# Optimization experiments

Measured on AMD Instinct MI355X. Metric: run time of the kernel, lower is better.

The kernel has to match this reference:

```python
import jax, jax.numpy as jnp
import numpy as np

COMMITMENT_COST = 0.25
NUM_EMBEDDINGS = 1024
EMBEDDING_DIM = 256


def setup_inputs() -> dict:
    key = jax.random.key(0)
    k1, k2 = jax.random.split(key)
    inputs = jax.random.normal(k1, (16, 4096, EMBEDDING_DIM), dtype=jnp.float32)
    # codebook initialized uniform(-1/K, 1/K) as in the torch module
    embeddings = jax.random.uniform(
        k2, (NUM_EMBEDDINGS, EMBEDDING_DIM), dtype=jnp.float32,
        minval=-1.0 / NUM_EMBEDDINGS, maxval=1.0 / NUM_EMBEDDINGS)
    return {"inputs": inputs, "embeddings": embeddings}


def reference(inputs, embeddings):
    sg = jax.lax.stop_gradient
    D = embeddings.shape[1]
    input_shape = inputs.shape
    flat = sg(inputs).reshape(-1, D)  # [N, D]
    distances = (jnp.sum(embeddings ** 2, axis=1)
                 + jnp.sum(flat ** 2, axis=1, keepdims=True)
                 - 2.0 * jnp.matmul(flat, embeddings.T))  # [N, K]
    indices = jnp.argmin(distances, axis=-1)  # [N]
    quantized = embeddings[indices].reshape(input_shape)
    e_latent_loss = jnp.mean((sg(quantized) - inputs) ** 2)
    q_latent_loss = jnp.mean((quantized - sg(inputs)) ** 2)
    loss = q_latent_loss + COMMITMENT_COST * e_latent_loss
    # straight-through estimator
    quantized = inputs + sg(quantized - inputs)
    return loss, quantized
```

## Files before the change

kernel.cpp:

```cpp
#include <hip/hip_runtime.h>
#include <math.h>

#define DIM 256
#define KCODES 1024
#define NTILE 64
#define BM 128
#define EB 4096.0f
#define UNIT_SCALE 0x7F7F7F7F

typedef __attribute__((ext_vector_type(8))) int i32x8;
typedef __attribute__((ext_vector_type(4))) int i32x4;
typedef __attribute__((ext_vector_type(4))) float f32x4;

__device__ inline unsigned fp4q(float v) {
  const float a = fabsf(v);
  const unsigned s = (v < 0.0f) ? 8u : 0u;
  unsigned m;
  if (a < 0.25f) m = 0;
  else if (a < 0.75f) m = 1;
  else if (a < 1.25f) m = 2;
  else if (a < 1.75f) m = 3;
  else if (a < 2.5f) m = 4;
  else if (a < 3.5f) m = 5;
  else if (a < 5.0f) m = 6;
  else m = 7;
  return s | m;
}

__global__ __launch_bounds__(64) void vq_prep_kernel(
    const float* __restrict__ E, float* __restrict__ enormh,
    unsigned char* __restrict__ Ef4) {
  const int k = blockIdx.x;
  const int t = threadIdx.x;
  const float4 v = *reinterpret_cast<const float4*>(&E[k * DIM + t * 4]);
  const int d0 = t * 4;
  const size_t byte = (size_t)((k >> 4) * 2048) + (size_t)((d0 >> 7) * 1024) +
                      (size_t)(((((d0 >> 5) & 3) * 16) + (k & 15)) * 16) +
                      (size_t)((d0 & 31) >> 1);
  const unsigned n0 = fp4q(v.x * EB), n1 = fp4q(v.y * EB);
  const unsigned n2 = fp4q(v.z * EB), n3 = fp4q(v.w * EB);
  const unsigned short pk =
      (unsigned short)(n0 | (n1 << 4) | (n2 << 8) | (n3 << 12));
  *reinterpret_cast<unsigned short*>(Ef4 + byte) = pk;
  float s = v.x * v.x + v.y * v.y + v.z * v.z + v.w * v.w;
#pragma unroll
  for (int off = 32; off >= 1; off >>= 1) s += __shfl_down(s, off);
  if (t == 0) enormh[k] = -0.5f * EB * s;
}

__global__ __launch_bounds__(256, 2) void vq_fused_kernel(
    const float* __restrict__ X, const float* __restrict__ E,
    const unsigned char* __restrict__ Ef4, const float* __restrict__ enormh,
    float* __restrict__ outq, float* __restrict__ partials) {
  __shared__ int idxs[BM];
  __shared__ float lred[4];

  const int tid = threadIdx.x;
  const int w = tid >> 6;
  const int lane = tid & 63;
  const int lr = lane & 15;
  const int lk = lane >> 4;
  const int row0 = blockIdx.x * BM;

  i32x8 Af[2][2];
  float xsq = 0.0f;
#pragma unroll
  for (int mt = 0; mt < 2; ++mt) {
    const float* xrow = &X[(size_t)(row0 + w * 32 + mt * 16 + lr) * DIM];
#pragma unroll
    for (int ks2 = 0; ks2 < 2; ++ks2) {
      const int k0 = ks2 * 128 + lk * 32;
      i32x8 af;
#pragma unroll
      for (int p = 0; p < 8; ++p) {
        const float4 a = *reinterpret_cast<const float4*>(&xrow[k0 + p * 4]);
        xsq += a.x * a.x + a.y * a.y + a.z * a.z + a.w * a.w;
        int pk = __builtin_amdgcn_cvt_pk_fp8_f32(a.x, a.y, 0, 0);
        pk = __builtin_amdgcn_cvt_pk_fp8_f32(a.z, a.w, pk, 1);
        af[p] = pk;
      }
      Af[mt][ks2] = af;
    }
  }

  float maxv[8];
  int mini[8];
#pragma unroll
  for (int i = 0; i < 8; ++i) { maxv[i] = -INFINITY; mini[i] = 0; }

  const char* efbase = reinterpret_cast<const char*>(Ef4) + lane * 16;

  i32x4 B0a, B0b, B1a, B1b;
  float en0, en1;
  B0a = *reinterpret_cast<const i32x4*>(efbase);
  B0b = *reinterpret_cast<const i32x4*>(efbase + 1024);
  B1a = *reinterpret_cast<const i32x4*>(efbase + 2048);
  B1b = *reinterpret_cast<const i32x4*>(efbase + 3072);
  en0 = enormh[lr];
  en1 = enormh[16 + lr];

#define COMPUTE_TILE(BA, BB)                                                  \
  {                                                                           \
    i32x8 ba8 = {}, bb8 = {};                                                 \
    ba8[0] = BA[0]; ba8[1] = BA[1]; ba8[2] = BA[2]; ba8[3] = BA[3];           \
    bb8[0] = BB[0]; bb8[1] = BB[1]; bb8[2] = BB[2]; bb8[3] = BB[3];           \
    acc0 = __builtin_amdgcn_mfma_scale_f32_16x16x128_f8f6f4(                  \
        Af[0][0], ba8, acc0, 0, 4, 0, UNIT_SCALE, 0, UNIT_SCALE);             \
    acc1 = __builtin_amdgcn_mfma_scale_f32_16x16x128_f8f6f4(                  \
        Af[1][0], ba8, acc1, 0, 4, 0, UNIT_SCALE, 0, UNIT_SCALE);             \
    acc0 = __builtin_amdgcn_mfma_scale_f32_16x16x128_f8f6f4(                  \
        Af[0][1], bb8, acc0, 0, 4, 0, UNIT_SCALE, 0, UNIT_SCALE);             \
    acc1 = __builtin_amdgcn_mfma_scale_f32_16x16x128_f8f6f4(                  \
        Af[1][1], bb8, acc1, 0, 4, 0, UNIT_SCALE, 0, UNIT_SCALE);             \
  }

#define RELOAD(BA, BB, EN, TILE)                                              \
  {                                                                           \
    const char* nsrc = efbase + (size_t)(TILE) * 2048;                        \
    BA = *reinterpret_cast<const i32x4*>(nsrc);                               \
    BB = *reinterpret_cast<const i32x4*>(nsrc + 1024);                        \
    EN = enormh[(TILE) * 16 + lr];                                            \
  }

#pragma unroll
  for (int t = 0; t < NTILE; ++t) {
    f32x4 acc0, acc1;
    if (t & 1) {
      acc0[0] = en1; acc0[1] = en1; acc0[2] = en1; acc0[3] = en1;
      acc1 = acc0;
      COMPUTE_TILE(B1a, B1b);
      if (t + 2 < NTILE) RELOAD(B1a, B1b, en1, t + 2);
    } else {
      acc0[0] = en0; acc0[1] = en0; acc0[2] = en0; acc0[3] = en0;
      acc1 = acc0;
      COMPUTE_TILE(B0a, B0b);
      if (t + 2 < NTILE) RELOAD(B0a, B0b, en0, t + 2);
    }
    const int code = t * 16 + lr;
#pragma unroll
    for (int r = 0; r < 4; ++r) {
      if (acc0[r] > maxv[r]) { maxv[r] = acc0[r]; mini[r] = code; }
      if (acc1[r] > maxv[4 + r]) { maxv[4 + r] = acc1[r]; mini[4 + r] = code; }
    }
  }
#undef COMPUTE_TILE
#undef RELOAD

#pragma unroll
  for (int off = 1; off < 16; off <<= 1) {
#pragma unroll
    for (int ri = 0; ri < 8; ++ri) {
      const float ov = __shfl_xor(maxv[ri], off);
      const int oi = __shfl_xor(mini[ri], off);
      if (ov > maxv[ri] || (ov == maxv[ri] && oi < mini[ri])) {
        maxv[ri] = ov; mini[ri] = oi;
      }
    }
  }
  if (lr == 0) {
#pragma unroll
    for (int mt = 0; mt < 2; ++mt)
#pragma unroll
      for (int r = 0; r < 4; ++r)
        idxs[w * 32 + mt * 16 + lk * 4 + r] = mini[mt * 4 + r];
  }

  float lsum = xsq;
  if (lr == 0) {
    float ssum = 0.0f;
#pragma unroll
    for (int ri = 0; ri < 8; ++ri) ssum += maxv[ri];
    lsum += ssum * (-2.0f / EB);
  }
#pragma unroll
  for (int off = 32; off >= 1; off >>= 1) lsum += __shfl_down(lsum, off);
  if (lane == 0) lred[w] = lsum;
  __syncthreads();

#pragma unroll
  for (int half = 0; half < 2; ++half) {
    const int er = half * 64 + (tid >> 2);
    const int eq = tid & 3;
    const int code = idxs[er];
    const float* erow = &E[(size_t)code * DIM];
    float* orow = &outq[(size_t)(row0 + er) * DIM];
#pragma unroll
    for (int j = 0; j < 16; ++j) {
      const int d = j * 16 + eq * 4;
      *reinterpret_cast<float4*>(&orow[d]) =
          *reinterpret_cast<const float4*>(&erow[d]);
    }
  }
  if (tid == 0)
    partials[blockIdx.x] = lred[0] + lred[1] + lred[2] + lred[3];
}

__global__ __launch_bounds__(256) void vq_finalize_kernel(
    const float* __restrict__ partials, float* __restrict__ out_loss,
    int nparts, float inv_count) {
  const int tid = threadIdx.x;
  float s = 0.0f;
  for (int i = tid; i < nparts; i += 256) s += partials[i];
#pragma unroll
  for (int off = 32; off >= 1; off >>= 1) s += __shfl_down(s, off);
  __shared__ float w[4];
  if ((tid & 63) == 0) w[tid >> 6] = s;
  __syncthreads();
  if (tid == 0)
    out_loss[0] = 1.25f * (w[0] + w[1] + w[2] + w[3]) * inv_count;
}

extern "C" void kernel_launch(void* const* d_in, const int* in_sizes, int n_in,
                              void* d_out, int out_size, void* d_ws,
                              size_t ws_size, hipStream_t stream) {
  const float* X = (const float*)d_in[0];
  const float* E = (const float*)d_in[1];
  float* out = (float*)d_out;

  char* ws = (char*)d_ws;
  float* enormh = (float*)ws;
  float* partials = (float*)(ws + 16 * 1024);
  unsigned char* Ef4 = (unsigned char*)(ws + 48 * 1024);

  const int nrows = in_sizes[0] / DIM;
  const int nb_main = nrows / BM;

  vq_prep_kernel<<<KCODES, 64, 0, stream>>>(E, enormh, Ef4);
  vq_fused_kernel<<<nb_main, 256, 0, stream>>>(X, E, Ef4, enormh, out + 1,
                                               partials);
  vq_finalize_kernel<<<1, 256, 0, stream>>>(partials, out, nb_main,
                                            1.0f / (float)in_sizes[0]);
}
```

Before: 51.36 us.

## Fuse loss finalize into main kernel via last-block counter and deepen B prefetch

Removes the separate finalize launch: each block publishes its partial loss, increments an atomic counter, and the last block to finish reduces all partials and writes the loss. The counter is reset in the prep kernel. The codebook tile prefetch also deepens from double to quad buffering to hide load latency in the MFMA loop. This adds register pressure and relies on threadfence ordering for correctness.

```diff
diff --git a/kernel.cpp b/kernel.cpp
--- a/kernel.cpp
+++ b/kernel.cpp
@@ -29,9 +29,10 @@
 
 __global__ __launch_bounds__(64) void vq_prep_kernel(
     const float* __restrict__ E, float* __restrict__ enormh,
-    unsigned char* __restrict__ Ef4) {
+    unsigned char* __restrict__ Ef4, unsigned int* __restrict__ counter) {
   const int k = blockIdx.x;
   const int t = threadIdx.x;
+  if (k == 0 && t == 0) counter[0] = 0u;
   const float4 v = *reinterpret_cast<const float4*>(&E[k * DIM + t * 4]);
   const int d0 = t * 4;
   const size_t byte = (size_t)((k >> 4) * 2048) + (size_t)((d0 >> 7) * 1024) +
@@ -51,9 +52,12 @@
 __global__ __launch_bounds__(256, 2) void vq_fused_kernel(
     const float* __restrict__ X, const float* __restrict__ E,
     const unsigned char* __restrict__ Ef4, const float* __restrict__ enormh,
-    float* __restrict__ outq, float* __restrict__ partials) {
+    float* __restrict__ outq, float* __restrict__ partials,
+    unsigned int* __restrict__ counter, float* __restrict__ out_loss,
+    int nblocks, float inv_count) {
   __shared__ int idxs[BM];
   __shared__ float lred[4];
+  __shared__ int last_flag;
 
   const int tid = threadIdx.x;
   const int w = tid >> 6;
@@ -90,51 +94,41 @@
 
   const char* efbase = reinterpret_cast<const char*>(Ef4) + lane * 16;
 
-  i32x4 B0a, B0b, B1a, B1b;
-  float en0, en1;
-  B0a = *reinterpret_cast<const i32x4*>(efbase);
-  B0b = *reinterpret_cast<const i32x4*>(efbase + 1024);
-  B1a = *reinterpret_cast<const i32x4*>(efbase + 2048);
-  B1b = *reinterpret_cast<const i32x4*>(efbase + 3072);
-  en0 = enormh[lr];
-  en1 = enormh[16 + lr];
-
-#define COMPUTE_TILE(BA, BB)                                                  \
-  {                                                                           \
-    i32x8 ba8 = {}, bb8 = {};                                                 \
-    ba8[0] = BA[0]; ba8[1] = BA[1]; ba8[2] = BA[2]; ba8[3] = BA[3];           \
-    bb8[0] = BB[0]; bb8[1] = BB[1]; bb8[2] = BB[2]; bb8[3] = BB[3];           \
-    acc0 = __builtin_amdgcn_mfma_scale_f32_16x16x128_f8f6f4(                  \
-        Af[0][0], ba8, acc0, 0, 4, 0, UNIT_SCALE, 0, UNIT_SCALE);             \
-    acc1 = __builtin_amdgcn_mfma_scale_f32_16x16x128_f8f6f4(                  \
-        Af[1][0], ba8, acc1, 0, 4, 0, UNIT_SCALE, 0, UNIT_SCALE);             \
-    acc0 = __builtin_amdgcn_mfma_scale_f32_16x16x128_f8f6f4(                  \
-        Af[0][1], bb8, acc0, 0, 4, 0, UNIT_SCALE, 0, UNIT_SCALE);             \
-    acc1 = __builtin_amdgcn_mfma_scale_f32_16x16x128_f8f6f4(                  \
-        Af[1][1], bb8, acc1, 0, 4, 0, UNIT_SCALE, 0, UNIT_SCALE);             \
-  }
-
-#define RELOAD(BA, BB, EN, TILE)                                              \
-  {                                                                           \
-    const char* nsrc = efbase + (size_t)(TILE) * 2048;                        \
-    BA = *reinterpret_cast<const i32x4*>(nsrc);                               \
-    BB = *reinterpret_cast<const i32x4*>(nsrc + 1024);                        \
-    EN = enormh[(TILE) * 16 + lr];                                            \
+  i32x4 Ba[4], Bb[4];
+  float en[4];
+#pragma unroll
+  for (int s = 0; s < 4; ++s) {
+    Ba[s] = *reinterpret_cast<const i32x4*>(efbase + (size_t)s * 2048);
+    Bb[s] = *reinterpret_cast<const i32x4*>(efbase + (size_t)s * 2048 + 1024);
+    en[s] = enormh[s * 16 + lr];
   }
 
 #pragma unroll
   for (int t = 0; t < NTILE; ++t) {
+    const int sl = t & 3;
     f32x4 acc0, acc1;
-    if (t & 1) {
-      acc0[0] = en1; acc0[1] = en1; acc0[2] = en1; acc0[3] = en1;
-      acc1 = acc0;
-      COMPUTE_TILE(B1a, B1b);
-      if (t + 2 < NTILE) RELOAD(B1a, B1b, en1, t + 2);
-    } else {
-      acc0[0] = en0; acc0[1] = en0; acc0[2] = en0; acc0[3] = en0;
-      acc1 = acc0;
-      COMPUTE_TILE(B0a, B0b);
-      if (t + 2 < NTILE) RELOAD(B0a, B0b, en0, t + 2);
+    acc0[0] = en[sl]; acc0[1] = en[sl]; acc0[2] = en[sl]; acc0[3] = en[sl];
+    acc1 = acc0;
+    {
+      i32x8 ba8 = {}, bb8 = {};
+      ba8[0] = Ba[sl][0]; ba8[1] = Ba[sl][1];
+      ba8[2] = Ba[sl][2]; ba8[3] = Ba[sl][3];
+      bb8[0] = Bb[sl][0]; bb8[1] = Bb[sl][1];
+      bb8[2] = Bb[sl][2]; bb8[3] = Bb[sl][3];
+      acc0 = __builtin_amdgcn_mfma_scale_f32_16x16x128_f8f6f4(
+          Af[0][0], ba8, acc0, 0, 4, 0, UNIT_SCALE, 0, UNIT_SCALE);
+      acc1 = __builtin_amdgcn_mfma_scale_f32_16x16x128_f8f6f4(
+          Af[1][0], ba8, acc1, 0, 4, 0, UNIT_SCALE, 0, UNIT_SCALE);
+      acc0 = __builtin_amdgcn_mfma_scale_f32_16x16x128_f8f6f4(
+          Af[0][1], bb8, acc0, 0, 4, 0, UNIT_SCALE, 0, UNIT_SCALE);
+      acc1 = __builtin_amdgcn_mfma_scale_f32_16x16x128_f8f6f4(
+          Af[1][1], bb8, acc1, 0, 4, 0, UNIT_SCALE, 0, UNIT_SCALE);
+    }
+    if (t + 4 < NTILE) {
+      const char* nsrc = efbase + (size_t)(t + 4) * 2048;
+      Ba[sl] = *reinterpret_cast<const i32x4*>(nsrc);
+      Bb[sl] = *reinterpret_cast<const i32x4*>(nsrc + 1024);
+      en[sl] = enormh[(t + 4) * 16 + lr];
     }
     const int code = t * 16 + lr;
 #pragma unroll
@@ -143,8 +137,6 @@
       if (acc1[r] > maxv[4 + r]) { maxv[4 + r] = acc1[r]; mini[4 + r] = code; }
     }
   }
-#undef COMPUTE_TILE
-#undef RELOAD
 
 #pragma unroll
   for (int off = 1; off < 16; off <<= 1) {
@@ -191,23 +183,27 @@
           *reinterpret_cast<const float4*>(&erow[d]);
     }
   }
-  if (tid == 0)
+
+  if (tid == 0) {
     partials[blockIdx.x] = lred[0] + lred[1] + lred[2] + lred[3];
-}
-
-__global__ __launch_bounds__(256) void vq_finalize_kernel(
-    const float* __restrict__ partials, float* __restrict__ out_loss,
-    int nparts, float inv_count) {
-  const int tid = threadIdx.x;
-  float s = 0.0f;
-  for (int i = tid; i < nparts; i += 256) s += partials[i];
-#pragma unroll
-  for (int off = 32; off >= 1; off >>= 1) s += __shfl_down(s, off);
-  __shared__ float w[4];
-  if ((tid & 63) == 0) w[tid >> 6] = s;
+    __threadfence();
+    const unsigned prev = atomicAdd(counter, 1u);
+    last_flag = (prev == (unsigned)(nblocks - 1)) ? 1 : 0;
+  }
   __syncthreads();
-  if (tid == 0)
-    out_loss[0] = 1.25f * (w[0] + w[1] + w[2] + w[3]) * inv_count;
+  if (last_flag) {
+    __threadfence();
+    const volatile float* vp = (const volatile float*)partials;
+    float s = 0.0f;
+    for (int i = tid; i < nblocks; i += 256) s += vp[i];
+#pragma unroll
+    for (int off = 32; off >= 1; off >>= 1) s += __shfl_down(s, off);
+    __shared__ float fw[4];
+    if ((tid & 63) == 0) fw[tid >> 6] = s;
+    __syncthreads();
+    if (tid == 0)
+      out_loss[0] = 1.25f * (fw[0] + fw[1] + fw[2] + fw[3]) * inv_count;
+  }
 }
 
 extern "C" void kernel_launch(void* const* d_in, const int* in_sizes, int n_in,
@@ -220,14 +216,14 @@
   char* ws = (char*)d_ws;
   float* enormh = (float*)ws;
   float* partials = (float*)(ws + 16 * 1024);
+  unsigned int* counter = (unsigned int*)(ws + 24 * 1024);
   unsigned char* Ef4 = (unsigned char*)(ws + 48 * 1024);
 
   const int nrows = in_sizes[0] / DIM;
   const int nb_main = nrows / BM;
 
-  vq_prep_kernel<<<KCODES, 64, 0, stream>>>(E, enormh, Ef4);
-  vq_fused_kernel<<<nb_main, 256, 0, stream>>>(X, E, Ef4, enormh, out + 1,
-                                               partials);
-  vq_finalize_kernel<<<1, 256, 0, stream>>>(partials, out, nb_main,
-                                            1.0f / (float)in_sizes[0]);
-}
+  vq_prep_kernel<<<KCODES, 64, 0, stream>>>(E, enormh, Ef4, counter);
+  vq_fused_kernel<<<nb_main, 256, 0, stream>>>(
+      X, E, Ef4, enormh, out + 1, partials, counter, out,
+      nb_main, 1.0f / (float)in_sizes[0]);
+}
```

After: 72.28 us. 1.41x slower.
